# Kernel optimization log

Hardware: AMD Instinct MI355X
Metric: run time of the kernel (lower is better)

The kernel has to match this reference:

```python
import jax, jax.numpy as jnp
import numpy as np

B, T, V, NH, HD = 2, 64, 32000, 32, 32  # head_dim == n_head required by the original einsum
C = NH * HD

def setup_inputs() -> dict:
    key = jax.random.key(0)
    k0, k1, k2 = jax.random.split(key, 3)
    return {
        "x": jax.random.normal(k0, (B, T, C), jnp.float32),
        "W_ffn": jax.random.normal(k1, (HD, HD), jnp.float32) / np.sqrt(HD),
        "b_ffn": jnp.zeros((HD,), jnp.float32),
        "temps": jnp.ones((NH,), jnp.float32),
        "vocab_emb": jax.random.normal(k2, (V, C), jnp.float32) * 0.02,
    }

def reference(x, W_ffn, b_ffn, temps, vocab_emb):
    b, t, c = x.shape
    nh = temps.shape[0]
    hd = c // nh
    v = vocab_emb.shape[0]
    # per-head channel FFN: Linear(head_dim, head_dim) with bias -> x @ W^T + b
    xc = x.reshape(b * t, nh, hd)
    ffn = jnp.einsum('bnh,dh->bnd', xc, W_ffn) + b_ffn  # (BT, nh, hd)
    # vocab channels: (nh, V, hd)
    vocab_ch = vocab_emb.reshape(v, nh, hd).transpose(1, 0, 2)
    # Original torch einsum 'bnh,hvd->bnv' contracts ffn's head_dim axis with
    # vocab_ch's n_head axis (equal sizes) AND sums over d. Mathematically this
    # equals contracting against vocab_sum[h, v] = sum_d vocab_ch[h, v, d].
    vocab_sum = vocab_ch.sum(-1)  # (nh==hd, V)
    logits = jnp.einsum('bnh,hv->bnv', ffn, vocab_sum)  # (BT, nh, V)
    temps_c = jnp.clip(temps, 0.1)[None, :, None]
    weights = jax.nn.softmax(logits / temps_c, axis=-1)
    # Original 'bnv,hvd->bnh' likewise sums d: out[b,n,h] = sum_v w[b,n,v]*vocab_sum[h,v]
    out = jnp.einsum('bnv,hv->bnh', weights, vocab_sum)  # (BT, nh, hd)
    return out.reshape(b, t, c)
```

## Files before the change

kernel.cpp:

```cpp
#include <hip/hip_runtime.h>
#include <hip/hip_bf16.h>

#define NV      32000
#define MROWS   4096
#define NSLICE  8
#define CHUNKS_PER_SLICE 125
#define PART_STRIDE 1056

typedef __attribute__((ext_vector_type(8))) short short8;
typedef __attribute__((ext_vector_type(16))) float f32x16;
typedef __attribute__((ext_vector_type(4))) float f32x4;

#define OFF_VSB  0
#define OFF_VSTB 2048000
#define OFF_FB   4096000
#define OFF_PART 4358144

#define NVS_BLOCKS 1000
#define NF_BLOCKS  512

static __device__ __forceinline__ unsigned pkbf(float lo, float hi) {
    union { __hip_bfloat162 h; unsigned u; } cv;
    cv.h.x = __float2bfloat16(lo);
    cv.h.y = __float2bfloat16(hi);
    return cv.u;
}
static __device__ __forceinline__ f32x4 ntload(const float* p) {
    return __builtin_nontemporal_load((const f32x4*)p);
}

__global__ __launch_bounds__(256)
void prep_kernel(const float* __restrict__ emb,
                 const float* __restrict__ x, const float* __restrict__ W,
                 const float* __restrict__ bias, const float* __restrict__ temps,
                 unsigned short* __restrict__ vsb,
                 unsigned short* __restrict__ vstb,
                 unsigned short* __restrict__ Fb) {
    const int blk = blockIdx.x;
    const int tid = threadIdx.x;
    if (blk < NVS_BLOCKS) {
        const int vbase = blk * 32;
        const int wave = tid >> 6, lane = tid & 63;
        __shared__ float lds[32][33];
        for (int vl = wave; vl < 32; vl += 4) {
            const float* p = emb + (size_t)(vbase + vl) * 1024 + lane * 4;
            f32x4 a0 = ntload(p), a1 = ntload(p + 256), a2 = ntload(p + 512), a3 = ntload(p + 768);
            float s0 = a0.x + a0.y + a0.z + a0.w;
            float s1 = a1.x + a1.y + a1.z + a1.w;
            float s2 = a2.x + a2.y + a2.z + a2.w;
            float s3 = a3.x + a3.y + a3.z + a3.w;
            s0 += __shfl_xor(s0, 1, 64); s0 += __shfl_xor(s0, 2, 64); s0 += __shfl_xor(s0, 4, 64);
            s1 += __shfl_xor(s1, 1, 64); s1 += __shfl_xor(s1, 2, 64); s1 += __shfl_xor(s1, 4, 64);
            s2 += __shfl_xor(s2, 1, 64); s2 += __shfl_xor(s2, 2, 64); s2 += __shfl_xor(s2, 4, 64);
            s3 += __shfl_xor(s3, 1, 64); s3 += __shfl_xor(s3, 2, 64); s3 += __shfl_xor(s3, 4, 64);
            if ((lane & 7) == 0) {
                int hb = lane >> 3;
                lds[vl][hb]      = s0;
                lds[vl][hb + 8]  = s1;
                lds[vl][hb + 16] = s2;
                lds[vl][hb + 24] = s3;
            }
        }
        __syncthreads();
        {
            int v = tid >> 3, h = (tid & 7) * 4;
            unsigned o[2];
            o[0] = pkbf(lds[v][h],     lds[v][h + 1]);
            o[1] = pkbf(lds[v][h + 2], lds[v][h + 3]);
            *(uint2*)(vsb + (size_t)(vbase + v) * 32 + h) = *(uint2*)o;
        }
        {
            int h = tid >> 3, vi = (tid & 7) * 4;
            unsigned o[2];
            o[0] = pkbf(lds[vi][h],     lds[vi + 1][h]);
            o[1] = pkbf(lds[vi + 2][h], lds[vi + 3][h]);
            *(uint2*)(vstb + (size_t)h * NV + vbase + vi) = *(uint2*)o;
        }
    } else {
        int t = (blk - NVS_BLOCKS) * 256 + tid;
        int frow = t >> 5, d = t & 31;
        const float4* xp = (const float4*)(x + (size_t)frow * 32);
        const float4* wp = (const float4*)(W + (size_t)d * 32);
        float s = bias[d];
#pragma unroll
        for (int i = 0; i < 8; ++i) {
            float4 xv = xp[i];
            float4 wv = wp[i];
            s += xv.x * wv.x + xv.y * wv.y + xv.z * wv.z + xv.w * wv.w;
        }
        float sc = 1.44269504088896f / fmaxf(temps[frow & 31], 0.1f);
        __hip_bfloat16 bv = __float2bfloat16(s * sc);
        Fb[t] = *reinterpret_cast<unsigned short*>(&bv);
    }
}

__global__ __launch_bounds__(256, 2)
void fused_mfma(const unsigned short* __restrict__ vsb,
                const unsigned short* __restrict__ vstb,
                const unsigned short* __restrict__ Fb,
                float* __restrict__ part) {
    const int b = blockIdx.x;
    const int s = b & 7;
    const int qp = b >> 3;
    const int tid = threadIdx.x;
    const int wave = tid >> 6, lane = tid & 63;
    const int hi = lane >> 5, c = lane & 31;

    const int qrow0 = qp * 64 + c;
    short8 q0a = *(const short8*)(Fb + (size_t)qrow0 * 32 + 8 * hi);
    short8 q0b = *(const short8*)(Fb + (size_t)qrow0 * 32 + 16 + 8 * hi);
    short8 q1a = *(const short8*)(Fb + (size_t)(qrow0 + 32) * 32 + 8 * hi);
    short8 q1b = *(const short8*)(Fb + (size_t)(qrow0 + 32) * 32 + 16 + 8 * hi);

    union { unsigned u[4]; short8 v8; } onesb;
    onesb.u[0] = 0x3F803F80u; onesb.u[1] = 0x3F803F80u;
    onesb.u[2] = 0x3F803F80u; onesb.u[3] = 0x3F803F80u;

    f32x16 oacc0, oacc1, lacc0, lacc1;
#pragma unroll
    for (int r = 0; r < 16; ++r) { oacc0[r] = 0.f; oacc1[r] = 0.f; lacc0[r] = 0.f; lacc1[r] = 0.f; }

    for (int ch = s * CHUNKS_PER_SLICE + wave; ch < (s + 1) * CHUNKS_PER_SLICE; ch += 4) {
        const int vbase = ch * 32;
        const unsigned short* vrow = vsb + (size_t)(vbase + c) * 32 + 8 * hi;
        short8 va0 = *(const short8*)(vrow);
        short8 va1 = *(const short8*)(vrow + 16);
        const unsigned short* vtrow = vstb + (size_t)c * NV + vbase + 8 * hi;
        short8 vb0 = *(const short8*)(vtrow);
        short8 vb1 = *(const short8*)(vtrow + 16);

#pragma unroll
        for (int t = 0; t < 2; ++t) {
            f32x16 sa;
#pragma unroll
            for (int r = 0; r < 16; ++r) sa[r] = 0.f;
            sa = __builtin_amdgcn_mfma_f32_32x32x16_bf16(va0, t ? q1a : q0a, sa, 0, 0, 0);
            sa = __builtin_amdgcn_mfma_f32_32x32x16_bf16(va1, t ? q1b : q0b, sa, 0, 0, 0);

            float w[16];
#pragma unroll
            for (int r = 0; r < 16; ++r) w[r] = __builtin_amdgcn_exp2f(sa[r]);

            unsigned u0 = pkbf(w[0], w[1]),   u1 = pkbf(w[2], w[3]);
            unsigned u2 = pkbf(w[4], w[5]),   u3 = pkbf(w[6], w[7]);
            unsigned u4 = pkbf(w[8], w[9]),   u5 = pkbf(w[10], w[11]);
            unsigned u6 = pkbf(w[12], w[13]), u7 = pkbf(w[14], w[15]);
            asm volatile("v_permlane32_swap_b32 %0, %1" : "+v"(u0), "+v"(u2));
            asm volatile("v_permlane32_swap_b32 %0, %1" : "+v"(u1), "+v"(u3));
            asm volatile("v_permlane32_swap_b32 %0, %1" : "+v"(u4), "+v"(u6));
            asm volatile("v_permlane32_swap_b32 %0, %1" : "+v"(u5), "+v"(u7));

            union { unsigned u[4]; short8 v8; } pa0, pa1;
            pa0.u[0] = u0; pa0.u[1] = u1; pa0.u[2] = u2; pa0.u[3] = u3;
            pa1.u[0] = u4; pa1.u[1] = u5; pa1.u[2] = u6; pa1.u[3] = u7;

            if (t == 0) {
                oacc0 = __builtin_amdgcn_mfma_f32_32x32x16_bf16(pa0.v8, vb0, oacc0, 0, 0, 0);
                oacc0 = __builtin_amdgcn_mfma_f32_32x32x16_bf16(pa1.v8, vb1, oacc0, 0, 0, 0);
                lacc0 = __builtin_amdgcn_mfma_f32_32x32x16_bf16(pa0.v8, onesb.v8, lacc0, 0, 0, 0);
                lacc0 = __builtin_amdgcn_mfma_f32_32x32x16_bf16(pa1.v8, onesb.v8, lacc0, 0, 0, 0);
            } else {
                oacc1 = __builtin_amdgcn_mfma_f32_32x32x16_bf16(pa0.v8, vb0, oacc1, 0, 0, 0);
                oacc1 = __builtin_amdgcn_mfma_f32_32x32x16_bf16(pa1.v8, vb1, oacc1, 0, 0, 0);
                lacc1 = __builtin_amdgcn_mfma_f32_32x32x16_bf16(pa0.v8, onesb.v8, lacc1, 0, 0, 0);
                lacc1 = __builtin_amdgcn_mfma_f32_32x32x16_bf16(pa1.v8, onesb.v8, lacc1, 0, 0, 0);
            }
        }
    }

    __shared__ float red[2][4][64 * 17];
    __shared__ float lred[2][4][32];
    {
        float* rw0 = &red[0][wave][lane * 17];
        float* rw1 = &red[1][wave][lane * 17];
#pragma unroll
        for (int r = 0; r < 16; ++r) { rw0[r] = oacc0[r]; rw1[r] = oacc1[r]; }
        if (c == 0) {
#pragma unroll
            for (int r = 0; r < 16; ++r) {
                int q = (r & 3) + 8 * (r >> 2) + 4 * hi;
                lred[0][wave][q] = lacc0[r];
                lred[1][wave][q] = lacc1[r];
            }
        }
    }
    __syncthreads();

#pragma unroll
    for (int t = 0; t < 2; ++t) {
        const size_t pbase = (size_t)((qp * 2 + t) * NSLICE + s) * PART_STRIDE;
        for (int idx = tid; idx < 1024; idx += 256) {
            int ln = idx >> 4, r = idx & 15;
            float sum = red[t][0][ln * 17 + r] + red[t][1][ln * 17 + r]
                      + red[t][2][ln * 17 + r] + red[t][3][ln * 17 + r];
            int lhi = ln >> 5, lc = ln & 31;
            int q = (r & 3) + 8 * (r >> 2) + 4 * lhi;
            part[pbase + (q << 5) + lc] = sum;
        }
        if (tid < 32)
            part[pbase + 1024 + tid] = lred[t][0][tid] + lred[t][1][tid]
                                     + lred[t][2][tid] + lred[t][3][tid];
    }
}

__global__ void combine_kernel(const float* __restrict__ part, float* __restrict__ out) {
    int t = blockIdx.x * 256 + threadIdx.x;
    if (t >= MROWS * 32) return;
    int qrow = t >> 5, j = t & 31;
    int qt = qrow >> 5, qi = qrow & 31;
    float a = 0.f, l = 0.f;
#pragma unroll
    for (int s = 0; s < NSLICE; ++s) {
        const float* p = part + (size_t)(qt * NSLICE + s) * PART_STRIDE;
        a += p[(qi << 5) + j];
        l += p[1024 + qi];
    }
    out[t] = a / l;
}

extern "C" void kernel_launch(void* const* d_in, const int* in_sizes, int n_in,
                              void* d_out, int out_size, void* d_ws, size_t ws_size,
                              hipStream_t stream) {
    const float* x     = (const float*)d_in[0];
    const float* W     = (const float*)d_in[1];
    const float* bias  = (const float*)d_in[2];
    const float* temps = (const float*)d_in[3];
    const float* emb   = (const float*)d_in[4];
    float* out = (float*)d_out;

    char* ws = (char*)d_ws;
    unsigned short* vsb  = (unsigned short*)(ws + OFF_VSB);
    unsigned short* vstb = (unsigned short*)(ws + OFF_VSTB);
    unsigned short* Fb   = (unsigned short*)(ws + OFF_FB);
    float*          part = (float*)(ws + OFF_PART);

    prep_kernel<<<NVS_BLOCKS + NF_BLOCKS, 256, 0, stream>>>(emb, x, W, bias, temps,
                                                            vsb, vstb, Fb);
    fused_mfma<<<64 * NSLICE, 256, 0, stream>>>(vsb, vstb, Fb, part);
    combine_kernel<<<(MROWS * 32 + 255) / 256, 256, 0, stream>>>(part, out);
}
```

Before: 62.34 us.

## Replace ones-MFMA row sums with VALU sums and double slice count

Computes the softmax denominator with VALU adds plus one cross-half shuffle instead of two extra MFMAs per tile against a ones matrix, removing a third of the matrix-core work in the inner loop. It also splits the vocabulary into 16 slices instead of 8, doubling the grid, and raises the launch-bounds occupancy hint from 2 to 4 blocks per CU. The extra slices mean twice as many partial results for the downstream combine, and the tighter register budget may cause spills. The row sum now uses the fp32 exp values rather than the bf16-rounded ones.

```diff
diff --git a/kernel.cpp b/kernel.cpp
--- a/kernel.cpp
+++ b/kernel.cpp
@@ -3,8 +3,7 @@
 
 #define NV      32000
 #define MROWS   4096
-#define NSLICE  8
-#define CHUNKS_PER_SLICE 125
+#define NSLICE  16
 #define PART_STRIDE 1056
 
 typedef __attribute__((ext_vector_type(8))) short short8;
@@ -94,14 +93,44 @@
     }
 }
 
-__global__ __launch_bounds__(256, 2)
+#define TILE(QA, QB, OACC, LSUM) do {                                              \
+    f32x16 sa;                                                                     \
+    _Pragma("unroll")                                                              \
+    for (int r = 0; r < 16; ++r) sa[r] = 0.f;                                      \
+    sa = __builtin_amdgcn_mfma_f32_32x32x16_bf16(va0, QA, sa, 0, 0, 0);            \
+    sa = __builtin_amdgcn_mfma_f32_32x32x16_bf16(va1, QB, sa, 0, 0, 0);            \
+    _Pragma("unroll")                                                              \
+    for (int r = 0; r < 16; ++r) sa[r] = __builtin_amdgcn_exp2f(sa[r]);            \
+    {                                                                              \
+        float t0 = sa[0] + sa[1],   t1 = sa[2] + sa[3];                            \
+        float t2 = sa[4] + sa[5],   t3 = sa[6] + sa[7];                            \
+        float t4 = sa[8] + sa[9],   t5 = sa[10] + sa[11];                          \
+        float t6 = sa[12] + sa[13], t7 = sa[14] + sa[15];                          \
+        LSUM += ((t0 + t1) + (t2 + t3)) + ((t4 + t5) + (t6 + t7));                 \
+    }                                                                              \
+    unsigned u0 = pkbf(sa[0], sa[1]),   u1 = pkbf(sa[2], sa[3]);                   \
+    unsigned u2 = pkbf(sa[4], sa[5]),   u3 = pkbf(sa[6], sa[7]);                   \
+    unsigned u4 = pkbf(sa[8], sa[9]),   u5 = pkbf(sa[10], sa[11]);                 \
+    unsigned u6 = pkbf(sa[12], sa[13]), u7 = pkbf(sa[14], sa[15]);                 \
+    asm volatile("v_permlane32_swap_b32 %0, %1" : "+v"(u0), "+v"(u2));             \
+    asm volatile("v_permlane32_swap_b32 %0, %1" : "+v"(u1), "+v"(u3));             \
+    asm volatile("v_permlane32_swap_b32 %0, %1" : "+v"(u4), "+v"(u6));             \
+    asm volatile("v_permlane32_swap_b32 %0, %1" : "+v"(u5), "+v"(u7));             \
+    union { unsigned u[4]; short8 v8; } pa0, pa1;                                  \
+    pa0.u[0] = u0; pa0.u[1] = u1; pa0.u[2] = u2; pa0.u[3] = u3;                    \
+    pa1.u[0] = u4; pa1.u[1] = u5; pa1.u[2] = u6; pa1.u[3] = u7;                    \
+    OACC = __builtin_amdgcn_mfma_f32_32x32x16_bf16(pa0.v8, vb0, OACC, 0, 0, 0);    \
+    OACC = __builtin_amdgcn_mfma_f32_32x32x16_bf16(pa1.v8, vb1, OACC, 0, 0, 0);    \
+} while (0)
+
+__global__ __launch_bounds__(256, 4)
 void fused_mfma(const unsigned short* __restrict__ vsb,
                 const unsigned short* __restrict__ vstb,
                 const unsigned short* __restrict__ Fb,
                 float* __restrict__ part) {
     const int b = blockIdx.x;
-    const int s = b & 7;
-    const int qp = b >> 3;
+    const int s = b & 15;
+    const int qp = b >> 4;
     const int tid = threadIdx.x;
     const int wave = tid >> 6, lane = tid & 63;
     const int hi = lane >> 5, c = lane & 31;
@@ -112,61 +141,29 @@
     short8 q1a = *(const short8*)(Fb + (size_t)(qrow0 + 32) * 32 + 8 * hi);
     short8 q1b = *(const short8*)(Fb + (size_t)(qrow0 + 32) * 32 + 16 + 8 * hi);
 
-    union { unsigned u[4]; short8 v8; } onesb;
-    onesb.u[0] = 0x3F803F80u; onesb.u[1] = 0x3F803F80u;
-    onesb.u[2] = 0x3F803F80u; onesb.u[3] = 0x3F803F80u;
-
-    f32x16 oacc0, oacc1, lacc0, lacc1;
-#pragma unroll
-    for (int r = 0; r < 16; ++r) { oacc0[r] = 0.f; oacc1[r] = 0.f; lacc0[r] = 0.f; lacc1[r] = 0.f; }
-
-    for (int ch = s * CHUNKS_PER_SLICE + wave; ch < (s + 1) * CHUNKS_PER_SLICE; ch += 4) {
-        const int vbase = ch * 32;
-        const unsigned short* vrow = vsb + (size_t)(vbase + c) * 32 + 8 * hi;
+    f32x16 oacc0, oacc1;
+#pragma unroll
+    for (int r = 0; r < 16; ++r) { oacc0[r] = 0.f; oacc1[r] = 0.f; }
+    float lsum0 = 0.f, lsum1 = 0.f;
+
+    const int c1 = (125 * (s + 1)) >> 1;
+    const unsigned short* vr_base = vsb + (c << 5) + (hi << 3);
+    const unsigned short* vt_base = vstb + (size_t)c * NV + (hi << 3);
+
+    for (int ch = ((125 * s) >> 1) + wave; ch < c1; ch += 4) {
+        const unsigned short* vrow = vr_base + ((size_t)ch << 10);
         short8 va0 = *(const short8*)(vrow);
         short8 va1 = *(const short8*)(vrow + 16);
-        const unsigned short* vtrow = vstb + (size_t)c * NV + vbase + 8 * hi;
+        const unsigned short* vtrow = vt_base + (ch << 5);
         short8 vb0 = *(const short8*)(vtrow);
         short8 vb1 = *(const short8*)(vtrow + 16);
 
-#pragma unroll
-        for (int t = 0; t < 2; ++t) {
-            f32x16 sa;
-#pragma unroll
-            for (int r = 0; r < 16; ++r) sa[r] = 0.f;
-            sa = __builtin_amdgcn_mfma_f32_32x32x16_bf16(va0, t ? q1a : q0a, sa, 0, 0, 0);
-            sa = __builtin_amdgcn_mfma_f32_32x32x16_bf16(va1, t ? q1b : q0b, sa, 0, 0, 0);
-
-            float w[16];
-#pragma unroll
-            for (int r = 0; r < 16; ++r) w[r] = __builtin_amdgcn_exp2f(sa[r]);
-
-            unsigned u0 = pkbf(w[0], w[1]),   u1 = pkbf(w[2], w[3]);
-            unsigned u2 = pkbf(w[4], w[5]),   u3 = pkbf(w[6], w[7]);
-            unsigned u4 = pkbf(w[8], w[9]),   u5 = pkbf(w[10], w[11]);
-            unsigned u6 = pkbf(w[12], w[13]), u7 = pkbf(w[14], w[15]);
-            asm volatile("v_permlane32_swap_b32 %0, %1" : "+v"(u0), "+v"(u2));
-            asm volatile("v_permlane32_swap_b32 %0, %1" : "+v"(u1), "+v"(u3));
-            asm volatile("v_permlane32_swap_b32 %0, %1" : "+v"(u4), "+v"(u6));
-            asm volatile("v_permlane32_swap_b32 %0, %1" : "+v"(u5), "+v"(u7));
-
-            union { unsigned u[4]; short8 v8; } pa0, pa1;
-            pa0.u[0] = u0; pa0.u[1] = u1; pa0.u[2] = u2; pa0.u[3] = u3;
-            pa1.u[0] = u4; pa1.u[1] = u5; pa1.u[2] = u6; pa1.u[3] = u7;
-
-            if (t == 0) {
-                oacc0 = __builtin_amdgcn_mfma_f32_32x32x16_bf16(pa0.v8, vb0, oacc0, 0, 0, 0);
-                oacc0 = __builtin_amdgcn_mfma_f32_32x32x16_bf16(pa1.v8, vb1, oacc0, 0, 0, 0);
-                lacc0 = __builtin_amdgcn_mfma_f32_32x32x16_bf16(pa0.v8, onesb.v8, lacc0, 0, 0, 0);
-                lacc0 = __builtin_amdgcn_mfma_f32_32x32x16_bf16(pa1.v8, onesb.v8, lacc0, 0, 0, 0);
-            } else {
-                oacc1 = __builtin_amdgcn_mfma_f32_32x32x16_bf16(pa0.v8, vb0, oacc1, 0, 0, 0);
-                oacc1 = __builtin_amdgcn_mfma_f32_32x32x16_bf16(pa1.v8, vb1, oacc1, 0, 0, 0);
-                lacc1 = __builtin_amdgcn_mfma_f32_32x32x16_bf16(pa0.v8, onesb.v8, lacc1, 0, 0, 0);
-                lacc1 = __builtin_amdgcn_mfma_f32_32x32x16_bf16(pa1.v8, onesb.v8, lacc1, 0, 0, 0);
-            }
-        }
-    }
+        TILE(q0a, q0b, oacc0, lsum0);
+        TILE(q1a, q1b, oacc1, lsum1);
+    }
+
+    lsum0 += __shfl_xor(lsum0, 32, 64);
+    lsum1 += __shfl_xor(lsum1, 32, 64);
 
     __shared__ float red[2][4][64 * 17];
     __shared__ float lred[2][4][32];
@@ -175,13 +172,9 @@
         float* rw1 = &red[1][wave][lane * 17];
 #pragma unroll
         for (int r = 0; r < 16; ++r) { rw0[r] = oacc0[r]; rw1[r] = oacc1[r]; }
-        if (c == 0) {
-#pragma unroll
-            for (int r = 0; r < 16; ++r) {
-                int q = (r & 3) + 8 * (r >> 2) + 4 * hi;
-                lred[0][wave][q] = lacc0[r];
-                lred[1][wave][q] = lacc1[r];
-            }
+        if (hi == 0) {
+            lred[0][wave][c] = lsum0;
+            lred[1][wave][c] = lsum1;
         }
     }
     __syncthreads();
```

New measurement: 62.11 us. Within noise of the previous version (-0.4%).
